# Kernel tuning notes

Hardware: AMD Instinct MI355X
Metric: run time of the kernel (lower is better)

The kernel has to match this reference:

```python
import jax, jax.numpy as jnp
import numpy as np

BN_EPS = 1e-3  # keras BatchNormalization default epsilon
NEG_INF = -1e30


def _masked_row_softmax(adjT):
    # tf.sparse.softmax semantics: softmax over NONZERO entries of each row;
    # implicit zeros stay exactly zero.
    mask = adjT != 0
    logits = jnp.where(mask, adjT, NEG_INF)
    p = jax.nn.softmax(logits, axis=-1)
    return jnp.where(mask, p, 0.0)


def _batch_norm(x, gamma, beta):
    # training-mode BN over all axes except channels
    mean = jnp.mean(x, axis=(0, 1), keepdims=True)
    var = jnp.var(x, axis=(0, 1), keepdims=True)
    return (x - mean) * jax.lax.rsqrt(var + BN_EPS) * gamma + beta


def setup_inputs() -> dict:
    key = jax.random.key(0)
    ks = jax.random.split(key, 4)
    B, N, F = 1, 8192, 128
    C0, C1 = 256, 128
    features = jax.random.normal(ks[0], (B, N, F), dtype=jnp.float32)
    adj = jax.random.randint(ks[1], (B, N, N), 0, 2, dtype=jnp.int32)
    kernel_1 = jax.random.normal(ks[2], (F, C0), dtype=jnp.float32) * (1.0 / np.sqrt(F))
    kernel_2 = jax.random.normal(ks[3], (C0, C1), dtype=jnp.float32) * (1.0 / np.sqrt(C0))
    return {
        "features": features,
        "adj": adj,
        "kernel_1": kernel_1,
        "bias_1": jnp.zeros((C0,), jnp.float32),
        "gamma_1": jnp.ones((C0,), jnp.float32),
        "beta_1": jnp.zeros((C0,), jnp.float32),
        "kernel_2": kernel_2,
        "bias_2": jnp.zeros((C1,), jnp.float32),
        "gamma_2": jnp.ones((C1,), jnp.float32),
        "beta_2": jnp.zeros((C1,), jnp.float32),
    }


def reference(features, adj, kernel_1, bias_1, gamma_1, beta_1,
              kernel_2, bias_2, gamma_2, beta_2):
    # fltr transposed: (B, Nr, Np), then sparse softmax over last dim
    adjT = jnp.transpose(adj.astype(jnp.float32), (0, 2, 1))
    w = _masked_row_softmax(adjT)                      # (B, Nr, Np)
    # people -> region aggregation + projection
    region = jnp.matmul(w, features)                   # (B, Nr, F)
    region = jnp.matmul(region, kernel_1) + bias_1     # (B, Nr, C0)
    region = _batch_norm(region, gamma_1, beta_1)
    # region -> people aggregation + projection
    people = jnp.matmul(jnp.transpose(w, (0, 2, 1)), region)  # (B, Np, C0)
    people = jnp.matmul(people, kernel_2) + bias_2             # (B, Np, C1)
    people = _batch_norm(people, gamma_2, beta_2)
    return people
```

## Files before the change

### kernel.cpp

```cpp
#include <hip/hip_runtime.h>
#include <stdint.h>

typedef unsigned int u32;
typedef unsigned short u16;
typedef __attribute__((ext_vector_type(8))) short short8;
typedef __attribute__((ext_vector_type(4))) float f32x4;

#define N8K 8192

__device__ __forceinline__ float b2f(u16 u) { return __uint_as_float(((u32)u) << 16); }
__device__ __forceinline__ u16 f2b(float f) {
  u32 i = __float_as_uint(f);
  i += 0x7FFFu + ((i >> 16) & 1u);
  return (u16)(i >> 16);
}
__device__ __forceinline__ u32 pk01(int x, int y) { return (u32)__mul24(x | (y << 16), 0x3F80); }
__device__ __forceinline__ u32 pkf(float a, float b) { return (u32)f2b(a) | ((u32)f2b(b) << 16); }

__device__ __forceinline__ void gl_lds16(const void* g, void* l) {
  __builtin_amdgcn_global_load_lds(
      (const __attribute__((address_space(1))) u32*)g,
      (__attribute__((address_space(3))) u32*)l, 16, 0, 0);
}

#define MFMA_4x4(As_, Bs_, aoff_, boff_)                                         \
  {                                                                              \
    short8 afr[4], bfr[4];                                                       \
    _Pragma("unroll") for (int i_ = 0; i_ < 4; ++i_)                             \
      afr[i_] = *(const short8*)(As_ + aoff_[i_]);                               \
    _Pragma("unroll") for (int j_ = 0; j_ < 4; ++j_)                             \
      bfr[j_] = *(const short8*)(Bs_ + boff_[j_]);                               \
    _Pragma("unroll") for (int i_ = 0; i_ < 4; ++i_)                             \
      _Pragma("unroll") for (int j_ = 0; j_ < 4; ++j_)                           \
        acc[i_][j_] = __builtin_amdgcn_mfma_f32_16x16x32_bf16(                   \
            afr[i_], bfr[j_], acc[i_][j_], 0, 0, 0);                             \
  }

#define ZERO_ACC()                                                               \
  f32x4 acc[4][4];                                                               \
  {                                                                              \
    const f32x4 fz = {0.f, 0.f, 0.f, 0.f};                                       \
    _Pragma("unroll") for (int i_ = 0; i_ < 4; ++i_)                             \
      _Pragma("unroll") for (int j_ = 0; j_ < 4; ++j_) acc[i_][j_] = fz;         \
  }

__global__ void k_detect(const u16* __restrict__ f16, int* __restrict__ flag) {
  __shared__ int cnt;
  if (threadIdx.x == 0) cnt = 0;
  __syncthreads();
  u16 u = f16[threadIdx.x * 2];
  int e = (u >> 7) & 0xFF;
  if (e >= 0x60 && e <= 0x9F) atomicAdd(&cnt, 1);
  __syncthreads();
  if (threadIdx.x == 0) *flag = (cnt >= 128) ? 1 : 0;
}

__global__ void k_prep(const void* __restrict__ featv, const void* __restrict__ K1v,
                       const void* __restrict__ K2v,
                       const void* __restrict__ b1v, const void* __restrict__ g1v,
                       const void* __restrict__ be1v, const void* __restrict__ b2v,
                       const void* __restrict__ g2v, const void* __restrict__ be2v,
                       const int* __restrict__ flagp,
                       u16* __restrict__ Ft, u16* __restrict__ K1T, u16* __restrict__ K2T,
                       float* __restrict__ deg, float* __restrict__ par,
                       float* __restrict__ bn1s, float* __restrict__ bn1q,
                       float* __restrict__ bn2s, float* __restrict__ bn2q) {
  const int b = blockIdx.x, t = threadIdx.x;
  const int flag = *flagp;
  if (b < 512) {
    int o = (b * 256 + t) << 3;
    int k0 = o >> 12, m = (o >> 5) & 127, kk = o & 31;
    uint4 w;
    if (flag) {
      const u16* s = (const u16*)featv + (size_t)(k0 * 32 + kk) * 128 + m;
      w.x = (u32)s[0]   | ((u32)s[128] << 16);
      w.y = (u32)s[256] | ((u32)s[384] << 16);
      w.z = (u32)s[512] | ((u32)s[640] << 16);
      w.w = (u32)s[768] | ((u32)s[896] << 16);
    } else {
      const float* s = (const float*)featv + (size_t)(k0 * 32 + kk) * 128 + m;
      w.x = pkf(s[0], s[128]); w.y = pkf(s[256], s[384]);
      w.z = pkf(s[512], s[640]); w.w = pkf(s[768], s[896]);
    }
    *(uint4*)(Ft + o) = w;
  } else if (b < 528) {
    int o = ((b - 512) * 256 + t) << 3;
    int k0 = o >> 13, c = (o >> 5) & 255, kk = o & 31;
    uint4 w;
    if (flag) {
      const u16* s = (const u16*)K1v + (size_t)(k0 * 32 + kk) * 256 + c;
      w.x = (u32)s[0]    | ((u32)s[256]  << 16);
      w.y = (u32)s[512]  | ((u32)s[768]  << 16);
      w.z = (u32)s[1024] | ((u32)s[1280] << 16);
      w.w = (u32)s[1536] | ((u32)s[1792] << 16);
    } else {
      const float* s = (const float*)K1v + (size_t)(k0 * 32 + kk) * 256 + c;
      w.x = pkf(s[0], s[256]); w.y = pkf(s[512], s[768]);
      w.z = pkf(s[1024], s[1280]); w.w = pkf(s[1536], s[1792]);
    }
    *(uint4*)(K1T + o) = w;
  } else if (b < 544) {
    int o = ((b - 528) * 256 + t) << 3;
    int k0 = o >> 12, c = (o >> 5) & 127, kk = o & 31;
    uint4 w;
    if (flag) {
      const u16* s = (const u16*)K2v + (size_t)(k0 * 32 + kk) * 128 + c;
      w.x = (u32)s[0]   | ((u32)s[128] << 16);
      w.y = (u32)s[256] | ((u32)s[384] << 16);
      w.z = (u32)s[512] | ((u32)s[640] << 16);
      w.w = (u32)s[768] | ((u32)s[896] << 16);
    } else {
      const float* s = (const float*)K2v + (size_t)(k0 * 32 + kk) * 128 + c;
      w.x = pkf(s[0], s[128]); w.y = pkf(s[256], s[384]);
      w.z = pkf(s[512], s[640]); w.w = pkf(s[768], s[896]);
    }
    *(uint4*)(K2T + o) = w;
  } else {
    if (t < 256) {
      par[t]       = flag ? b2f(((const u16*)b1v)[t])  : ((const float*)b1v)[t];
      par[256 + t] = flag ? b2f(((const u16*)g1v)[t])  : ((const float*)g1v)[t];
      par[512 + t] = flag ? b2f(((const u16*)be1v)[t]) : ((const float*)be1v)[t];
      bn1s[t] = 0.f; bn1q[t] = 0.f;
    }
    if (t < 128) {
      par[768 + t]  = flag ? b2f(((const u16*)b2v)[t])  : ((const float*)b2v)[t];
      par[896 + t]  = flag ? b2f(((const u16*)g2v)[t])  : ((const float*)g2v)[t];
      par[1024 + t] = flag ? b2f(((const u16*)be2v)[t]) : ((const float*)be2v)[t];
      bn2s[t] = 0.f; bn2q[t] = 0.f;
    }
    for (int i = t; i < N8K; i += 256) deg[i] = 0.f;
  }
}

__global__ __launch_bounds__(256, 2)
void k_gemm1(const int* __restrict__ adj, const u16* __restrict__ Ft,
             float* __restrict__ P1, float* __restrict__ deg, int ksteps) {
  __shared__ __align__(16) u16 As[128 * 32];
  __shared__ __align__(16) u16 Bs[128 * 32];
  __shared__ float degp[128];
  const int t = threadIdx.x, bx = blockIdx.x;
  const int nt = bx & 63, s = bx >> 6;
  const int n0 = nt << 7;
  const int lane = t & 63, wv = t >> 6;
  const int wm = (wv & 1) << 6, wn = (wv >> 1) << 6;
  const int fm = lane & 15, fq = lane >> 4;
  if (t < 128) degp[t] = 0.0f;
  ZERO_ACC();
  int aoff[4], boff[4];
#pragma unroll
  for (int i = 0; i < 4; ++i) aoff[i] = (wm + i * 16 + fm) * 32 + fq * 8;
#pragma unroll
  for (int j = 0; j < 4; ++j) {
    int n = wn + j * 16 + fm;
    boff[j] = n * 32 + ((fq * 8) ^ (((n >> 2) & 3) << 3));
  }
  const int rb = t & 31, kb = t >> 5;
  const int* gB = adj + ((size_t)s * ksteps * 32 + kb * 4) * N8K + n0 + rb * 4;
  const char* gA = (const char*)(Ft + (size_t)s * ksteps * 4096);
  char* lA = (char*)As + ((t >> 6) << 10);
  const int goff = t << 4;
  u16* lb = Bs + (rb * 4) * 32 + ((kb * 4) ^ ((rb & 3) << 3));
  int ds0 = 0, ds1 = 0, ds2 = 0, ds3 = 0;
  for (int ks = 0; ks < ksteps; ++ks) {
    __syncthreads();
    gl_lds16(gA + goff, lA);
    gl_lds16(gA + 4096 + goff, lA + 4096);
    int4 a0 = *(const int4*)(gB);
    int4 a1 = *(const int4*)(gB + N8K);
    int4 a2 = *(const int4*)(gB + 2 * N8K);
    int4 a3 = *(const int4*)(gB + 3 * N8K);
    gA += 8192;
    gB += 32 * N8K;
    ds0 += a0.x + a1.x + a2.x + a3.x;
    ds1 += a0.y + a1.y + a2.y + a3.y;
    ds2 += a0.z + a1.z + a2.z + a3.z;
    ds3 += a0.w + a1.w + a2.w + a3.w;
    uint2 w;
    w.x = pk01(a0.x, a1.x); w.y = pk01(a2.x, a3.x); *(uint2*)(lb) = w;
    w.x = pk01(a0.y, a1.y); w.y = pk01(a2.y, a3.y); *(uint2*)(lb + 32) = w;
    w.x = pk01(a0.z, a1.z); w.y = pk01(a2.z, a3.z); *(uint2*)(lb + 64) = w;
    w.x = pk01(a0.w, a1.w); w.y = pk01(a2.w, a3.w); *(uint2*)(lb + 96) = w;
    __syncthreads();
    MFMA_4x4(As, Bs, aoff, boff);
  }
  atomicAdd(&degp[rb * 4 + 0], (float)ds0);
  atomicAdd(&degp[rb * 4 + 1], (float)ds1);
  atomicAdd(&degp[rb * 4 + 2], (float)ds2);
  atomicAdd(&degp[rb * 4 + 3], (float)ds3);
  float* base = P1 + ((size_t)s * N8K + n0) * 128;
#pragma unroll
  for (int i = 0; i < 4; ++i)
#pragma unroll
    for (int j = 0; j < 4; ++j) {
      int r = wn + j * 16 + fm;
      int f = wm + i * 16 + fq * 4;
      *(f32x4*)(base + (size_t)r * 128 + f) = acc[i][j];
    }
  __syncthreads();
  if (t < 128) atomicAdd(&deg[n0 + t], degp[t]);
}

__global__ __launch_bounds__(256, 2)
void k_projf(const float* __restrict__ Psrc, const float* __restrict__ deg,
             const u16* __restrict__ Bt, const float* __restrict__ bias,
             float* __restrict__ Cout, float* __restrict__ bns, float* __restrict__ bnq,
             int nsplit, int ksteps, int Ncols, int useinv) {
  __shared__ __align__(16) u16 As[128 * 32];
  __shared__ __align__(16) u16 Bs[128 * 32];
  const int t = threadIdx.x, bx = blockIdx.x;
  const int mt = bx & 63, ct = bx >> 6;
  const int m0 = mt << 7, n0 = ct << 7;
  const int lane = t & 63, wv = t >> 6;
  const int wm = (wv & 1) << 6, wn = (wv >> 1) << 6;
  const int fm = lane & 15, fq = lane >> 4;
  const int K = ksteps << 5;
  ZERO_ACC();
  int aoff[4], boff[4];
#pragma unroll
  for (int i = 0; i < 4; ++i) {
    int m = wm + i * 16 + fm;
    aoff[i] = m * 32 + ((fq * 8) ^ (((m >> 2) & 3) << 3));
  }
#pragma unroll
  for (int j = 0; j < 4; ++j) boff[j] = (wn + j * 16 + fm) * 32 + fq * 8;
  const int row = t >> 1;
  const size_t sstride = (size_t)N8K * K;
  const float* src = Psrc + (size_t)(m0 + row) * K + (t & 1) * 16;
  float inv = 1.0f;
  if (useinv) {
    float d = deg[m0 + row];
    inv = (d > 0.5f) ? 1.0f / d : 0.0f;
  }
  const int swzA = ((t >> 3) & 3) << 3;
  u16* la0 = As + row * 32 + (((t & 1) * 16) ^ swzA);
  u16* la1 = As + row * 32 + ((((t & 1) * 16) + 8) ^ swzA);
  char* lB = (char*)Bs + ((t >> 6) << 10);
  const int goff = t << 4;
  for (int ks = 0; ks < ksteps; ++ks) {
    __syncthreads();
    const char* gB = (const char*)(Bt + ((size_t)ks * Ncols + n0) * 32);
    gl_lds16(gB + goff, lB);
    gl_lds16(gB + 4096 + goff, lB + 4096);
    f32x4 s0 = {0.f, 0.f, 0.f, 0.f}, s1 = s0, s2 = s0, s3 = s0;
    const float* p = src + ks * 32;
    for (int sp = 0; sp < nsplit; ++sp) {
      const f32x4* q = (const f32x4*)(p + sp * sstride);
      s0 += q[0]; s1 += q[1]; s2 += q[2]; s3 += q[3];
    }
    s0 *= inv; s1 *= inv; s2 *= inv; s3 *= inv;
    uint4 w;
    w.x = pkf(s0[0], s0[1]); w.y = pkf(s0[2], s0[3]);
    w.z = pkf(s1[0], s1[1]); w.w = pkf(s1[2], s1[3]);
    *(uint4*)la0 = w;
    w.x = pkf(s2[0], s2[1]); w.y = pkf(s2[2], s2[3]);
    w.z = pkf(s3[0], s3[1]); w.w = pkf(s3[2], s3[3]);
    *(uint4*)la1 = w;
    __syncthreads();
    MFMA_4x4(As, Bs, aoff, boff);
  }
#pragma unroll
  for (int j = 0; j < 4; ++j) {
    int c = n0 + wn + j * 16 + fm;
    float bc = bias[c];
    float t1 = 0.f, t2 = 0.f;
#pragma unroll
    for (int i = 0; i < 4; ++i) {
      int r = m0 + wm + i * 16 + fq * 4;
#pragma unroll
      for (int ii = 0; ii < 4; ++ii) {
        float v = acc[i][j][ii] + bc;
        Cout[(size_t)(r + ii) * Ncols + c] = v;
        t1 += v; t2 += v * v;
      }
    }
    t1 += __shfl_xor(t1, 16); t1 += __shfl_xor(t1, 32);
    t2 += __shfl_xor(t2, 16); t2 += __shfl_xor(t2, 32);
    if (fq == 0) { atomicAdd(&bns[c], t1); atomicAdd(&bnq[c], t2); }
  }
}

__global__ void k_bn1apply(const float* __restrict__ region1, const float* __restrict__ deg,
                           const float* __restrict__ bn1s, const float* __restrict__ bn1q,
                           const float* __restrict__ g1, const float* __restrict__ be1,
                           u16* __restrict__ RsT) {
  const int blk = blockIdx.x;
  const int t = threadIdx.x;
  const int r0 = blk << 5;
  const int cg = (t & 63) << 2;
  const int rg0 = (t >> 6) << 2;
  float scale[4], shift[4];
#pragma unroll
  for (int jj = 0; jj < 4; ++jj) {
    int c = cg + jj;
    float mu = bn1s[c] * (1.0f / 8192.0f);
    float var = bn1q[c] * (1.0f / 8192.0f) - mu * mu;
    float inv = rsqrtf(var + 1e-3f);
    scale[jj] = inv * g1[c];
    shift[jj] = be1[c] - mu * scale[jj];
  }
#pragma unroll
  for (int half = 0; half < 2; ++half) {
    int rg = rg0 + (half << 4);
    f32x4 x[4]; float idg[4];
#pragma unroll
    for (int i = 0; i < 4; ++i) {
      int r = r0 + rg + i;
      x[i] = *(const f32x4*)(region1 + (size_t)r * 256 + cg);
      float d = deg[r];
      idg[i] = (d > 0.5f) ? 1.0f / d : 0.0f;
    }
#pragma unroll
    for (int jj = 0; jj < 4; ++jj) {
      int c = cg + jj;
      float y0 = (x[0][jj] * scale[jj] + shift[jj]) * idg[0];
      float y1 = (x[1][jj] * scale[jj] + shift[jj]) * idg[1];
      float y2 = (x[2][jj] * scale[jj] + shift[jj]) * idg[2];
      float y3 = (x[3][jj] * scale[jj] + shift[jj]) * idg[3];
      uint2 w;
      w.x = pkf(y0, y1);
      w.y = pkf(y2, y3);
      *(uint2*)(RsT + (size_t)blk * 8192 + (size_t)c * 32 + rg) = w;
    }
  }
}

__global__ __launch_bounds__(256, 2)
void k_gemm2(const int* __restrict__ adj, const u16* __restrict__ RsT,
             float* __restrict__ P2, int ksteps) {
  __shared__ __align__(16) u16 As[128 * 32];
  __shared__ __align__(16) u16 Bs[128 * 32];
  const int t = threadIdx.x, bx = blockIdx.x;
  const int mt = bx & 63, ct = (bx >> 6) & 1, s = bx >> 7;
  const int m0 = mt << 7, n0 = ct << 7;
  const int lane = t & 63, wv = t >> 6;
  const int wm = (wv & 1) << 6, wn = (wv >> 1) << 6;
  const int fm = lane & 15, fq = lane >> 4;
  ZERO_ACC();
  int aoff[4], boff[4];
#pragma unroll
  for (int i = 0; i < 4; ++i) {
    int m = wm + i * 16 + fm;
    aoff[i] = m * 32 + ((fq * 8) ^ (((m >> 2) & 3) << 3));
  }
#pragma unroll
  for (int j = 0; j < 4; ++j) boff[j] = (wn + j * 16 + fm) * 32 + fq * 8;
  const int* gA = adj + (size_t)(m0 + (t >> 1)) * N8K + (size_t)s * ksteps * 32 + (t & 1) * 16;
  const char* gB = (const char*)(RsT + ((size_t)s * ksteps * 256 + n0) * 32);
  char* lB = (char*)Bs + ((t >> 6) << 10);
  const int goff = t << 4;
  const int swzA = ((t >> 3) & 3) << 3;
  u16* la0 = As + (t >> 1) * 32 + (((t & 1) * 16) ^ swzA);
  u16* la1 = As + (t >> 1) * 32 + ((((t & 1) * 16) + 8) ^ swzA);
  for (int ks = 0; ks < ksteps; ++ks) {
    __syncthreads();
    gl_lds16(gB + goff, lB);
    gl_lds16(gB + 4096 + goff, lB + 4096);
    int4 a0 = *(const int4*)(gA);
    int4 a1 = *(const int4*)(gA + 4);
    int4 a2 = *(const int4*)(gA + 8);
    int4 a3 = *(const int4*)(gA + 12);
    gA += 32;
    gB += 16384;
    uint4 w;
    w.x = pk01(a0.x, a0.y); w.y = pk01(a0.z, a0.w);
    w.z = pk01(a1.x, a1.y); w.w = pk01(a1.z, a1.w);
    *(uint4*)la0 = w;
    w.x = pk01(a2.x, a2.y); w.y = pk01(a2.z, a2.w);
    w.z = pk01(a3.x, a3.y); w.w = pk01(a3.z, a3.w);
    *(uint4*)la1 = w;
    __syncthreads();
    MFMA_4x4(As, Bs, aoff, boff);
  }
  float* base = P2 + (size_t)s * N8K * 256;
#pragma unroll
  for (int i = 0; i < 4; ++i)
#pragma unroll
    for (int j = 0; j < 4; ++j) {
      int c = n0 + wn + j * 16 + fm;
      int pr = m0 + wm + i * 16 + fq * 4;
#pragma unroll
      for (int ii = 0; ii < 4; ++ii)
        base[(size_t)(pr + ii) * 256 + c] = acc[i][j][ii];
    }
}

__global__ void k_bn2apply(const float* __restrict__ people1,
                           const float* __restrict__ bn2s, const float* __restrict__ bn2q,
                           const float* __restrict__ g2, const float* __restrict__ be2,
                           void* __restrict__ outv, const int* __restrict__ flagp) {
  int g = blockIdx.x * 256 + threadIdx.x;
  int p = g >> 5;
  int c = (g & 31) << 2;
  f32x4 x = *(const f32x4*)(people1 + (size_t)p * 128 + c);
  f32x4 y;
#pragma unroll
  for (int jj = 0; jj < 4; ++jj) {
    int cc = c + jj;
    float mu = bn2s[cc] * (1.0f / 8192.0f);
    float var = bn2q[cc] * (1.0f / 8192.0f) - mu * mu;
    float inv = rsqrtf(var + 1e-3f);
    y[jj] = (x[jj] - mu) * inv * g2[cc] + be2[cc];
  }
  if (*flagp) {
    uint2 w;
    w.x = pkf(y[0], y[1]);
    w.y = pkf(y[2], y[3]);
    *(uint2*)((u16*)outv + (size_t)p * 128 + c) = w;
  } else {
    *(f32x4*)((float*)outv + (size_t)p * 128 + c) = y;
  }
}

extern "C" void kernel_launch(void* const* d_in, const int* in_sizes, int n_in,
                              void* d_out, int out_size, void* d_ws, size_t ws_size,
                              hipStream_t stream) {
  const void* feat = d_in[0];
  const int* adj   = (const int*)d_in[1];
  const void* K1   = d_in[2];
  const void* b1   = d_in[3];
  const void* g1   = d_in[4];
  const void* be1  = d_in[5];
  const void* K2   = d_in[6];
  const void* b2   = d_in[7];
  const void* g2   = d_in[8];
  const void* be2  = d_in[9];
  char* ws = (char*)d_ws;
  const size_t MB = 1u << 20;

  float* Pbig    = (float*)(ws);
  float* region1 = (float*)(ws + 32 * MB);
  float* people1 = (float*)(ws + 40 * MB);
  u16*   Ft      = (u16*)(ws + 44 * MB);
  u16*   RsT     = (u16*)(ws + 46 * MB);
  u16*   K1T     = (u16*)(ws + 50 * MB);
  u16*   K2T     = K1T + 32768;
  float* deg     = (float*)(K2T + 32768);
  float* par     = deg + N8K;
  float* bn1s    = par + 1152;
  float* bn1q    = bn1s + 256;
  float* bn2s    = bn1q + 256;
  float* bn2q    = bn2s + 128;
  int*   flag    = (int*)(bn2q + 128);

  k_detect<<<1, 256, 0, stream>>>((const u16*)feat, flag);
  k_prep<<<545, 256, 0, stream>>>(feat, K1, K2, b1, g1, be1, b2, g2, be2, flag,
                                  Ft, K1T, K2T, deg, par, bn1s, bn1q, bn2s, bn2q);
  k_gemm1<<<512, 256, 0, stream>>>(adj, Ft, Pbig, deg, 32);
  k_projf<<<128, 256, 0, stream>>>(Pbig, deg, K1T, par + 0, region1, bn1s, bn1q,
                                   8, 4, 256, 1);
  k_bn1apply<<<256, 256, 0, stream>>>(region1, deg, bn1s, bn1q, par + 256, par + 512, RsT);
  k_gemm2<<<512, 256, 0, stream>>>(adj, RsT, Pbig, 64);
  k_projf<<<64, 256, 0, stream>>>(Pbig, deg, K2T, par + 768, people1, bn2s, bn2q,
                                  4, 8, 128, 0);
  k_bn2apply<<<1024, 256, 0, stream>>>(people1, bn2s, bn2q, par + 896, par + 1024,
                                       d_out, flag);
}
```

Measured before the change: 528.1 us.

## Reassociate second aggregation to project by K2 before adjacency GEMM

The BN1-normalized region features are multiplied by K2 first (new k_bnH kernel), so the second adjacency GEMM runs over 128 columns instead of 256. That halves its MFMA work and its partial-sum traffic. A small reduction kernel then sums the split-K partials, adds the bias and accumulates BN2 statistics. The format-detect kernel is folded into k_prep and k_bn2apply as a block vote, the feature transpose now goes through LDS for coalesced access, and k_projf's block ordering is changed. Exchanges: an extra bf16 rounding of the intermediate H, and the vote is recomputed in every block.

```diff
diff --git a/kernel.cpp b/kernel.cpp
--- a/kernel.cpp
+++ b/kernel.cpp
@@ -16,6 +16,12 @@
 }
 __device__ __forceinline__ u32 pk01(int x, int y) { return (u32)__mul24(x | (y << 16), 0x3F80); }
 __device__ __forceinline__ u32 pkf(float a, float b) { return (u32)f2b(a) | ((u32)f2b(b) << 16); }
+
+__device__ __forceinline__ int dvote(const u16* f16) {
+  u16 u = f16[threadIdx.x * 2];
+  int e = (u >> 7) & 0xFF;
+  return __syncthreads_count((e >= 0x60 && e <= 0x9F) ? 1 : 0) >= 128;
+}
 
 __device__ __forceinline__ void gl_lds16(const void* g, void* l) {
   __builtin_amdgcn_global_load_lds(
@@ -44,47 +50,47 @@
       _Pragma("unroll") for (int j_ = 0; j_ < 4; ++j_) acc[i_][j_] = fz;         \
   }
 
-__global__ void k_detect(const u16* __restrict__ f16, int* __restrict__ flag) {
-  __shared__ int cnt;
-  if (threadIdx.x == 0) cnt = 0;
-  __syncthreads();
-  u16 u = f16[threadIdx.x * 2];
-  int e = (u >> 7) & 0xFF;
-  if (e >= 0x60 && e <= 0x9F) atomicAdd(&cnt, 1);
-  __syncthreads();
-  if (threadIdx.x == 0) *flag = (cnt >= 128) ? 1 : 0;
-}
-
 __global__ void k_prep(const void* __restrict__ featv, const void* __restrict__ K1v,
                        const void* __restrict__ K2v,
                        const void* __restrict__ b1v, const void* __restrict__ g1v,
                        const void* __restrict__ be1v, const void* __restrict__ b2v,
                        const void* __restrict__ g2v, const void* __restrict__ be2v,
-                       const int* __restrict__ flagp,
                        u16* __restrict__ Ft, u16* __restrict__ K1T, u16* __restrict__ K2T,
                        float* __restrict__ deg, float* __restrict__ par,
                        float* __restrict__ bn1s, float* __restrict__ bn1q,
                        float* __restrict__ bn2s, float* __restrict__ bn2q) {
   const int b = blockIdx.x, t = threadIdx.x;
-  const int flag = *flagp;
-  if (b < 512) {
-    int o = (b * 256 + t) << 3;
-    int k0 = o >> 12, m = (o >> 5) & 127, kk = o & 31;
-    uint4 w;
+  const int flag = dvote((const u16*)featv);
+  if (b < 256) {
+    __shared__ __align__(16) u16 Ls[32 * 136];
+    const int pr = t >> 3, ck = t & 7;
+    u16 v[16];
     if (flag) {
-      const u16* s = (const u16*)featv + (size_t)(k0 * 32 + kk) * 128 + m;
-      w.x = (u32)s[0]   | ((u32)s[128] << 16);
-      w.y = (u32)s[256] | ((u32)s[384] << 16);
-      w.z = (u32)s[512] | ((u32)s[640] << 16);
-      w.w = (u32)s[768] | ((u32)s[896] << 16);
+      const u16* s = (const u16*)featv + (size_t)(b * 32 + pr) * 128 + ck * 16;
+      uint4 a = *(const uint4*)(s);
+      uint4 bq = *(const uint4*)(s + 8);
+      *(uint4*)&v[0] = a; *(uint4*)&v[8] = bq;
     } else {
-      const float* s = (const float*)featv + (size_t)(k0 * 32 + kk) * 128 + m;
-      w.x = pkf(s[0], s[128]); w.y = pkf(s[256], s[384]);
-      w.z = pkf(s[512], s[640]); w.w = pkf(s[768], s[896]);
-    }
-    *(uint4*)(Ft + o) = w;
-  } else if (b < 528) {
-    int o = ((b - 512) * 256 + t) << 3;
+      const float* s = (const float*)featv + (size_t)(b * 32 + pr) * 128 + ck * 16;
+#pragma unroll
+      for (int i = 0; i < 16; ++i) v[i] = f2b(s[i]);
+    }
+    *(uint4*)(Ls + pr * 136 + ck * 16) = *(uint4*)&v[0];
+    *(uint4*)(Ls + pr * 136 + ck * 16 + 8) = *(uint4*)&v[8];
+    __syncthreads();
+    const int f = t >> 1, h16 = (t & 1) * 16;
+    u32 w[8];
+#pragma unroll
+    for (int i = 0; i < 8; ++i) {
+      u16 lo = Ls[(h16 + 2 * i) * 136 + f];
+      u16 hi = Ls[(h16 + 2 * i + 1) * 136 + f];
+      w[i] = (u32)lo | ((u32)hi << 16);
+    }
+    u16* d = Ft + (size_t)b * 4096 + f * 32 + h16;
+    *(uint4*)(d) = *(uint4*)&w[0];
+    *(uint4*)(d + 8) = *(uint4*)&w[4];
+  } else if (b < 272) {
+    int o = ((b - 256) * 256 + t) << 3;
     int k0 = o >> 13, c = (o >> 5) & 255, kk = o & 31;
     uint4 w;
     if (flag) {
@@ -99,8 +105,8 @@
       w.z = pkf(s[1024], s[1280]); w.w = pkf(s[1536], s[1792]);
     }
     *(uint4*)(K1T + o) = w;
-  } else if (b < 544) {
-    int o = ((b - 528) * 256 + t) << 3;
+  } else if (b < 288) {
+    int o = ((b - 272) * 256 + t) << 3;
     int k0 = o >> 12, c = (o >> 5) & 127, kk = o & 31;
     uint4 w;
     if (flag) {
@@ -208,7 +214,7 @@
   __shared__ __align__(16) u16 As[128 * 32];
   __shared__ __align__(16) u16 Bs[128 * 32];
   const int t = threadIdx.x, bx = blockIdx.x;
-  const int mt = bx & 63, ct = bx >> 6;
+  const int ct = bx & 1, mt = (bx >> 1) & 63;
   const int m0 = mt << 7, n0 = ct << 7;
   const int lane = t & 63, wv = t >> 6;
   const int wm = (wv & 1) << 6, wn = (wv >> 1) << 6;
@@ -279,59 +285,91 @@
   }
 }
 
-__global__ void k_bn1apply(const float* __restrict__ region1, const float* __restrict__ deg,
-                           const float* __restrict__ bn1s, const float* __restrict__ bn1q,
-                           const float* __restrict__ g1, const float* __restrict__ be1,
-                           u16* __restrict__ RsT) {
-  const int blk = blockIdx.x;
-  const int t = threadIdx.x;
-  const int r0 = blk << 5;
-  const int cg = (t & 63) << 2;
-  const int rg0 = (t >> 6) << 2;
-  float scale[4], shift[4];
-#pragma unroll
-  for (int jj = 0; jj < 4; ++jj) {
-    int c = cg + jj;
-    float mu = bn1s[c] * (1.0f / 8192.0f);
-    float var = bn1q[c] * (1.0f / 8192.0f) - mu * mu;
-    float inv = rsqrtf(var + 1e-3f);
-    scale[jj] = inv * g1[c];
-    shift[jj] = be1[c] - mu * scale[jj];
-  }
-#pragma unroll
-  for (int half = 0; half < 2; ++half) {
-    int rg = rg0 + (half << 4);
-    f32x4 x[4]; float idg[4];
-#pragma unroll
-    for (int i = 0; i < 4; ++i) {
-      int r = r0 + rg + i;
-      x[i] = *(const f32x4*)(region1 + (size_t)r * 256 + cg);
-      float d = deg[r];
-      idg[i] = (d > 0.5f) ? 1.0f / d : 0.0f;
-    }
-#pragma unroll
-    for (int jj = 0; jj < 4; ++jj) {
-      int c = cg + jj;
-      float y0 = (x[0][jj] * scale[jj] + shift[jj]) * idg[0];
-      float y1 = (x[1][jj] * scale[jj] + shift[jj]) * idg[1];
-      float y2 = (x[2][jj] * scale[jj] + shift[jj]) * idg[2];
-      float y3 = (x[3][jj] * scale[jj] + shift[jj]) * idg[3];
+__global__ __launch_bounds__(256, 2)
+void k_bnH(const float* __restrict__ region1, const float* __restrict__ deg,
+           const float* __restrict__ bn1s, const float* __restrict__ bn1q,
+           const float* __restrict__ g1, const float* __restrict__ be1,
+           const u16* __restrict__ K2T, u16* __restrict__ HT) {
+  __shared__ __align__(16) u16 As[128 * 32];
+  __shared__ __align__(16) u16 Bs[128 * 32];
+  __shared__ float scS[256], shS[256];
+  const int t = threadIdx.x, mt = blockIdx.x;
+  const int m0 = mt << 7;
+  const int lane = t & 63, wv = t >> 6;
+  const int wm = (wv & 1) << 6, wn = (wv >> 1) << 6;
+  const int fm = lane & 15, fq = lane >> 4;
+  {
+    float mu = bn1s[t] * (1.0f / 8192.0f);
+    float var = bn1q[t] * (1.0f / 8192.0f) - mu * mu;
+    float iv = rsqrtf(var + 1e-3f);
+    float sc = iv * g1[t];
+    scS[t] = sc;
+    shS[t] = be1[t] - mu * sc;
+  }
+  ZERO_ACC();
+  int aoff[4], boff[4];
+#pragma unroll
+  for (int i = 0; i < 4; ++i) {
+    int m = wm + i * 16 + fm;
+    aoff[i] = m * 32 + ((fq * 8) ^ (((m >> 2) & 3) << 3));
+  }
+#pragma unroll
+  for (int j = 0; j < 4; ++j) boff[j] = (wn + j * 16 + fm) * 32 + fq * 8;
+  const int row = t >> 1, half = t & 1;
+  float d = deg[m0 + row];
+  const float idg = (d > 0.5f) ? 1.0f / d : 0.0f;
+  const float* src = region1 + (size_t)(m0 + row) * 256 + half * 16;
+  const int swzA = ((t >> 3) & 3) << 3;
+  u16* la0 = As + row * 32 + ((half * 16) ^ swzA);
+  u16* la1 = As + row * 32 + (((half * 16) + 8) ^ swzA);
+  char* lB = (char*)Bs + ((t >> 6) << 10);
+  const int goff = t << 4;
+  for (int ks = 0; ks < 8; ++ks) {
+    __syncthreads();
+    const char* gB = (const char*)(K2T + (size_t)ks * 4096);
+    gl_lds16(gB + goff, lB);
+    gl_lds16(gB + 4096 + goff, lB + 4096);
+    const float* p = src + ks * 32;
+    const int cb = ks * 32 + half * 16;
+    float y[16];
+#pragma unroll
+    for (int q = 0; q < 4; ++q) {
+      f32x4 x = *(const f32x4*)(p + q * 4);
+#pragma unroll
+      for (int jj = 0; jj < 4; ++jj)
+        y[q * 4 + jj] = (x[jj] * scS[cb + q * 4 + jj] + shS[cb + q * 4 + jj]) * idg;
+    }
+    uint4 w;
+    w.x = pkf(y[0], y[1]); w.y = pkf(y[2], y[3]);
+    w.z = pkf(y[4], y[5]); w.w = pkf(y[6], y[7]);
+    *(uint4*)la0 = w;
+    w.x = pkf(y[8], y[9]); w.y = pkf(y[10], y[11]);
+    w.z = pkf(y[12], y[13]); w.w = pkf(y[14], y[15]);
+    *(uint4*)la1 = w;
+    __syncthreads();
+    MFMA_4x4(As, Bs, aoff, boff);
+  }
+#pragma unroll
+  for (int i = 0; i < 4; ++i)
+#pragma unroll
+    for (int j = 0; j < 4; ++j) {
+      int c = wn + j * 16 + fm;
+      int r = m0 + wm + i * 16 + fq * 4;
       uint2 w;
-      w.x = pkf(y0, y1);
-      w.y = pkf(y2, y3);
-      *(uint2*)(RsT + (size_t)blk * 8192 + (size_t)c * 32 + rg) = w;
-    }
-  }
+      w.x = pkf(acc[i][j][0], acc[i][j][1]);
+      w.y = pkf(acc[i][j][2], acc[i][j][3]);
+      *(uint2*)(HT + (size_t)(r >> 5) * 4096 + c * 32 + (r & 31)) = w;
+    }
 }
 
 __global__ __launch_bounds__(256, 2)
-void k_gemm2(const int* __restrict__ adj, const u16* __restrict__ RsT,
+void k_gemm2(const int* __restrict__ adj, const u16* __restrict__ HT,
              float* __restrict__ P2, int ksteps) {
   __shared__ __align__(16) u16 As[128 * 32];
   __shared__ __align__(16) u16 Bs[128 * 32];
   const int t = threadIdx.x, bx = blockIdx.x;
-  const int mt = bx & 63, ct = (bx >> 6) & 1, s = bx >> 7;
-  const int m0 = mt << 7, n0 = ct << 7;
+  const int mt = bx & 63, s = bx >> 6;
+  const int m0 = mt << 7;
   const int lane = t & 63, wv = t >> 6;
   const int wm = (wv & 1) << 6, wn = (wv >> 1) << 6;
   const int fm = lane & 15, fq = lane >> 4;
@@ -344,13 +382,14 @@
   }
 #pragma unroll
   for (int j = 0; j < 4; ++j) boff[j] = (wn + j * 16 + fm) * 32 + fq * 8;
-  const int* gA = adj + (size_t)(m0 + (t >> 1)) * N8K + (size_t)s * ksteps * 32 + (t & 1) * 16;
-  const char* gB = (const char*)(RsT + ((size_t)s * ksteps * 256 + n0) * 32);
+  const int row = t >> 1, half = t & 1;
+  const int* gA = adj + (size_t)(m0 + row) * N8K + (size_t)s * ksteps * 32 + half * 16;
+  const char* gB = (const char*)(HT + (size_t)s * ksteps * 4096);
   char* lB = (char*)Bs + ((t >> 6) << 10);
   const int goff = t << 4;
   const int swzA = ((t >> 3) & 3) << 3;
-  u16* la0 = As + (t >> 1) * 32 + (((t & 1) * 16) ^ swzA);
-  u16* la1 = As + (t >> 1) * 32 + ((((t & 1) * 16) + 8) ^ swzA);
+  u16* la0 = As + row * 32 + ((half * 16) ^ swzA);
+  u16* la1 = As + row * 32 + (((half * 16) + 8) ^ swzA);
   for (int ks = 0; ks < ksteps; ++ks) {
     __syncthreads();
     gl_lds16(gB + goff, lB);
@@ -360,7 +399,7 @@
     int4 a2 = *(const int4*)(gA + 8);
     int4 a3 = *(const int4*)(gA + 12);
     gA += 32;
-    gB += 16384;
+    gB += 8192;
     uint4 w;
     w.x = pk01(a0.x, a0.y); w.y = pk01(a0.z, a0.w);
     w.z = pk01(a1.x, a1.y); w.w = pk01(a1.z, a1.w);
@@ -371,23 +410,49 @@
     __syncthreads();
     MFMA_4x4(As, Bs, aoff, boff);
   }
-  float* base = P2 + (size_t)s * N8K * 256;
+  float* base = P2 + (size_t)s * N8K * 128;
 #pragma unroll
   for (int i = 0; i < 4; ++i)
 #pragma unroll
     for (int j = 0; j < 4; ++j) {
-      int c = n0 + wn + j * 16 + fm;
+      int c = wn + j * 16 + fm;
       int pr = m0 + wm + i * 16 + fq * 4;
 #pragma unroll
       for (int ii = 0; ii < 4; ++ii)
-        base[(size_t)(pr + ii) * 256 + c] = acc[i][j][ii];
-    }
+        base[(size_t)(pr + ii) * 128 + c] = acc[i][j][ii];
+    }
+}
+
+__global__ void k_red2(const float* __restrict__ P2, const float* __restrict__ bias,
+                       float* __restrict__ people1,
+                       float* __restrict__ bn2s, float* __restrict__ bn2q) {
+  __shared__ float r1[256], r2[256];
+  const int t = threadIdx.x;
+  const int c = t & 127, pg = t >> 7;
+  const int p0 = blockIdx.x << 5;
+  const float bc = bias[c];
+  float s1 = 0.f, s2 = 0.f;
+  for (int pp = pg; pp < 32; pp += 2) {
+    size_t o = (size_t)(p0 + pp) * 128 + c;
+    float v = bc;
+#pragma unroll
+    for (int s = 0; s < 8; ++s) v += P2[(size_t)s * N8K * 128 + o];
+    people1[o] = v;
+    s1 += v; s2 += v * v;
+  }
+  r1[t] = s1; r2[t] = s2;
+  __syncthreads();
+  if (t < 128) {
+    atomicAdd(&bn2s[t], r1[t] + r1[t + 128]);
+    atomicAdd(&bn2q[t], r2[t] + r2[t + 128]);
+  }
 }
 
 __global__ void k_bn2apply(const float* __restrict__ people1,
                            const float* __restrict__ bn2s, const float* __restrict__ bn2q,
                            const float* __restrict__ g2, const float* __restrict__ be2,
-                           void* __restrict__ outv, const int* __restrict__ flagp) {
+                           const u16* __restrict__ featprobe, void* __restrict__ outv) {
+  const int flag = dvote(featprobe);
   int g = blockIdx.x * 256 + threadIdx.x;
   int p = g >> 5;
   int c = (g & 31) << 2;
@@ -401,7 +466,7 @@
     float inv = rsqrtf(var + 1e-3f);
     y[jj] = (x[jj] - mu) * inv * g2[cc] + be2[cc];
   }
-  if (*flagp) {
+  if (flag) {
     uint2 w;
     w.x = pkf(y[0], y[1]);
     w.y = pkf(y[2], y[3]);
@@ -431,8 +496,8 @@
   float* region1 = (float*)(ws + 32 * MB);
   float* people1 = (float*)(ws + 40 * MB);
   u16*   Ft      = (u16*)(ws + 44 * MB);
-  u16*   RsT     = (u16*)(ws + 46 * MB);
-  u16*   K1T     = (u16*)(ws + 50 * MB);
+  u16*   HT      = (u16*)(ws + 46 * MB);
+  u16*   K1T     = (u16*)(ws + 48 * MB);
   u16*   K2T     = K1T + 32768;
   float* deg     = (float*)(K2T + 32768);
   float* par     = deg + N8K;
@@ -440,18 +505,16 @@
   float* bn1q    = bn1s + 256;
   float* bn2s    = bn1q + 256;
   float* bn2q    = bn2s + 128;
-  int*   flag    = (int*)(bn2q + 128);
-
-  k_detect<<<1, 256, 0, stream>>>((const u16*)feat, flag);
-  k_prep<<<545, 256, 0, stream>>>(feat, K1, K2, b1, g1, be1, b2, g2, be2, flag,
+
+  k_prep<<<289, 256, 0, stream>>>(feat, K1, K2, b1, g1, be1, b2, g2, be2,
                                   Ft, K1T, K2T, deg, par, bn1s, bn1q, bn2s, bn2q);
   k_gemm1<<<512, 256, 0, stream>>>(adj, Ft, Pbig, deg, 32);
   k_projf<<<128, 256, 0, stream>>>(Pbig, deg, K1T, par + 0, region1, bn1s, bn1q,
                                    8, 4, 256, 1);
-  k_bn1apply<<<256, 256, 0, stream>>>(region1, deg, bn1s, bn1q, par + 256, par + 512, RsT);
-  k_gemm2<<<512, 256, 0, stream>>>(adj, RsT, Pbig, 64);
-  k_projf<<<64, 256, 0, stream>>>(Pbig, deg, K2T, par + 768, people1, bn2s, bn2q,
-                                  4, 8, 128, 0);
+  k_bnH<<<64, 256, 0, stream>>>(region1, deg, bn1s, bn1q, par + 256, par + 512,
+                                K2T, HT);
+  k_gemm2<<<512, 256, 0, stream>>>(adj, HT, Pbig, 32);
+  k_red2<<<256, 256, 0, stream>>>(Pbig, par + 768, people1, bn2s, bn2q);
   k_bn2apply<<<1024, 256, 0, stream>>>(people1, bn2s, bn2q, par + 896, par + 1024,
-                                       d_out, flag);
-}
+                                       (const u16*)feat, d_out);
+}
```

After: 497.6 us. -5.8%, faster.
